# Kernel tuning notes

Measured on AMD Instinct MI355X. Metric: run time of the kernel, lower is better.

Reference implementation:

```python
import jax, jax.numpy as jnp
import numpy as np

N = 50000      # nodes (single coalesced node type)
IN = 256       # in_dim
H = 8          # attention heads
D = 64         # hidden_dim (per-head out dim)
HD = H * D     # 512, fused feature dim
OUT = 64       # final out_dim
M = 2          # meta-paths
E = 800000     # edges per meta-path graph
SEM_HID = 128  # SemanticAttention hidden size (DGL/OpenHGNN default)
NEG_SLOPE = 0.2


def setup_inputs() -> dict:
    key = jax.random.key(0)
    ks = jax.random.split(key, 13)
    s = 0.05
    return {
        "x": jax.random.normal(ks[0], (N, IN), jnp.float32),
        "src": jax.random.randint(ks[1], (M, E), 0, N, jnp.int32),
        "dst": jax.random.randint(ks[2], (M, E), 0, N, jnp.int32),
        # per-metapath GATConv params
        "Wg": jax.random.normal(ks[3], (M, IN, HD), jnp.float32) * s,
        "al": jax.random.normal(ks[4], (M, H, D), jnp.float32) * s,
        "ar": jax.random.normal(ks[5], (M, H, D), jnp.float32) * s,
        "bg": jax.random.normal(ks[6], (M, HD), jnp.float32) * s,
        # semantic attention: Linear(HD,128) -> tanh -> Linear(128,1,no bias)
        "W1": jax.random.normal(ks[7], (HD, SEM_HID), jnp.float32) * s,
        "b1": jax.random.normal(ks[8], (SEM_HID,), jnp.float32) * s,
        "q": jax.random.normal(ks[9], (SEM_HID,), jnp.float32) * s,
        # final linear
        "Wout": jax.random.normal(ks[10], (HD, OUT), jnp.float32) * s,
        "bout": jax.random.normal(ks[11], (OUT,), jnp.float32) * s,
    }


def _gat(x, W, al, ar, b, src, dst):
    # x: [N, IN] -> feat: [N, H, D]
    feat = (x @ W).reshape(N, H, D)
    el = jnp.sum(feat * al, axis=-1)                      # [N, H]
    er = jnp.sum(feat * ar, axis=-1)                      # [N, H]
    e = jax.nn.leaky_relu(el[src] + er[dst], NEG_SLOPE)   # [E, H]
    # edge softmax per destination node (allow zero in-degree)
    m = jax.ops.segment_max(e, dst, num_segments=N)       # [N, H]
    m = jnp.where(jnp.isfinite(m), m, 0.0)
    ex = jnp.exp(e - m[dst])                              # [E, H]
    den = jax.ops.segment_sum(ex, dst, num_segments=N)    # [N, H]
    alpha = ex / jnp.maximum(den[dst], 1e-9)              # [E, H]
    # scatter-aggregate messages: [E, H, D] -> [N, H, D]
    out = jax.ops.segment_sum(alpha[:, :, None] * feat[src], dst, num_segments=N)
    return jax.nn.elu(out.reshape(N, HD) + b)             # flatten heads + bias + elu


def reference(x, src, dst, Wg, al, ar, bg, W1, b1, q, Wout, bout):
    # per-metapath GAT (loop over M=2 structurally distinct graphs)
    zs = [_gat(x, Wg[p], al[p], ar[p], bg[p], src[p], dst[p]) for p in range(M)]
    z = jnp.stack(zs, axis=1)                             # [N, M, HD]
    # semantic attention fusion
    w = jnp.mean(jnp.tanh(z @ W1 + b1) @ q, axis=0)       # [M]
    beta = jax.nn.softmax(w)                              # [M]
    fused = jnp.einsum("nmf,m->nf", z, beta)             # [N, HD]
    # final linear
    return fused @ Wout + bout                            # [N, OUT]
```

## Files before the change

### kernel.cpp

```cpp
#include <hip/hip_runtime.h>
#include <cstdint>

#define N_NODES 50000
#define IN_DIM 256
#define H_HEADS 8
#define D_HEAD 64
#define HD 512
#define OUT_DIM 64
#define M_PATHS 2
#define E_EDGES 800000
#define SEM_HID 128
#define NEG_SLOPE 0.2f
#define ELL_CAP 64
#define ELX_BLOCKS 782

typedef __attribute__((ext_vector_type(8))) short bf16x8;
typedef __attribute__((ext_vector_type(4))) float f32x4;
typedef __attribute__((ext_vector_type(8))) unsigned short u16x8;

__device__ __forceinline__ float b2f(unsigned short u) {
  return __uint_as_float(((unsigned)u) << 16);
}
__device__ __forceinline__ unsigned short f2b(float f) {
  unsigned u = __float_as_uint(f);
  unsigned r = (u + 0x7fffu + ((u >> 16) & 1u)) >> 16;
  return (unsigned short)r;
}

__device__ __forceinline__ float eluf(float x) {
  return x > 0.f ? x : (expf(x) - 1.f);
}
__device__ __forceinline__ float lrelu(float x) {
  return x > 0.f ? x : NEG_SLOPE * x;
}

__global__ void k_prep(const float* __restrict__ Wg, const float* __restrict__ W1,
                       const float* __restrict__ Wout, const float* __restrict__ al,
                       const float* __restrict__ ar,
                       unsigned short* __restrict__ WgbT, unsigned short* __restrict__ W1T,
                       unsigned short* __restrict__ WoutT, unsigned short* __restrict__ WALR,
                       int* __restrict__ deg2, float* __restrict__ wsem) {
  int gid = blockIdx.x * blockDim.x + threadIdx.x;
  if (gid < 262144) {
    int m = gid >> 17, r = gid & 131071, n = r >> 8, k = r & 255;
    WgbT[(size_t)m * 131072 + n * 256 + k] = f2b(Wg[(size_t)m * 131072 + k * 512 + n]);
  } else if (gid < 327680) {
    int r = gid - 262144; int c = r >> 9, k = r & 511;
    W1T[c * 512 + k] = f2b(W1[k * 128 + c]);
  } else if (gid < 360448) {
    int r = gid - 327680; int c = r >> 9, k = r & 511;
    WoutT[c * 512 + k] = f2b(Wout[k * 64 + c]);
  } else if (gid < 368640) {
    int r = gid - 360448;
    int c = r >> 8, k = r & 255;
    int m = c >> 4, side = (c >> 3) & 1, h = c & 7;
    const float* av = (side ? ar : al) + m * HD + h * D_HEAD;
    const float* wrow = Wg + (size_t)m * 131072 + (size_t)k * HD + h * D_HEAD;
    float s = 0.f;
#pragma unroll
    for (int d = 0; d < 64; ++d) s += wrow[d] * av[d];
    WALR[c * 256 + k] = f2b(s);
  } else if (gid < 468640) {
    deg2[gid - 368640] = 0;
  } else if (gid < 468642) {
    wsem[gid - 468640] = 0.f;
  }
}

__global__ __launch_bounds__(256) void k_elx_edge(const float* __restrict__ xfp,
                                                  const unsigned short* __restrict__ WALR,
                                                  unsigned short* __restrict__ xb,
                                                  float* __restrict__ el2,
                                                  float* __restrict__ er2,
                                                  const int* __restrict__ src0,
                                                  const int* __restrict__ dst0,
                                                  int* __restrict__ deg0,
                                                  unsigned short* __restrict__ ell) {
  __shared__ __align__(16) unsigned short As[64][72];
  __shared__ __align__(16) unsigned short Bs[32][72];
  const int tid = threadIdx.x;
  if (blockIdx.x >= ELX_BLOCKS) {
    int e = (blockIdx.x - ELX_BLOCKS) * 256 + tid;
    if (e < E_EDGES) {
      int d = dst0[e];
      int p = atomicAdd(&deg0[d], 1);
      if (p < ELL_CAP) ell[d * ELL_CAP + p] = (unsigned short)src0[e];
    }
    return;
  }
  const int r0 = blockIdx.x * 64;
  const int w = tid >> 6, lane = tid & 63;
  const int cl = lane & 15, kg = lane >> 4;
  f32x4 acc[2] = {};
  for (int k0 = 0; k0 < IN_DIM; k0 += 64) {
#pragma unroll
    for (int p = 0; p < 2; ++p) {
      int idx = tid + p * 256;
      int row = idx >> 3, ko = (idx & 7) * 8;
      u16x8 v = (u16x8)(unsigned short)0;
      int grow = r0 + row;
      if (grow < N_NODES) {
        const float4* g = (const float4*)&xfp[(size_t)grow * IN_DIM + k0 + ko];
        float4 g0 = g[0], g1 = g[1];
        v[0] = f2b(g0.x); v[1] = f2b(g0.y); v[2] = f2b(g0.z); v[3] = f2b(g0.w);
        v[4] = f2b(g1.x); v[5] = f2b(g1.y); v[6] = f2b(g1.z); v[7] = f2b(g1.w);
        *(u16x8*)&xb[(size_t)grow * IN_DIM + k0 + ko] = v;
      }
      *(u16x8*)&As[row][ko] = v;
    }
    {
      int col = tid >> 3, ko = (tid & 7) * 8;
      *(u16x8*)&Bs[col][ko] = *(const u16x8*)&WALR[col * 256 + k0 + ko];
    }
    __syncthreads();
#pragma unroll
    for (int kk = 0; kk < 64; kk += 32) {
      bf16x8 a = *(const bf16x8*)&As[w * 16 + cl][kk + kg * 8];
#pragma unroll
      for (int ct = 0; ct < 2; ++ct) {
        bf16x8 b = *(const bf16x8*)&Bs[ct * 16 + cl][kk + kg * 8];
        acc[ct] = __builtin_amdgcn_mfma_f32_16x16x32_bf16(a, b, acc[ct], 0, 0, 0);
      }
    }
    __syncthreads();
  }
#pragma unroll
  for (int ct = 0; ct < 2; ++ct) {
    int col = ct * 16 + cl;
    int m = col >> 4, side = (col >> 3) & 1, h = col & 7;
    float* dstp = (side ? er2 : el2) + m * 400000;
#pragma unroll
    for (int reg = 0; reg < 4; ++reg) {
      int row = r0 + w * 16 + kg * 4 + reg;
      if (row < N_NODES) dstp[row * 8 + h] = acc[ct][reg];
    }
  }
}

__global__ void k_edge_e(const int* __restrict__ src, const int* __restrict__ dst,
                         int* __restrict__ deg, unsigned short* __restrict__ ell_src) {
  int e = blockIdx.x * blockDim.x + threadIdx.x;
  if (e >= E_EDGES) return;
  int d = dst[e];
  int p = atomicAdd(&deg[d], 1);
  if (p < ELL_CAP) ell_src[d * ELL_CAP + p] = (unsigned short)src[e];
}

__global__ __launch_bounds__(256) void k_gemm_feat(const unsigned short* __restrict__ xb,
                                                   const unsigned short* __restrict__ BT,
                                                   unsigned short* __restrict__ C) {
  __shared__ __align__(16) unsigned short As[64][72];
  __shared__ __align__(16) unsigned short Bs[256][72];
  const int tid = threadIdx.x;
  const int r0 = blockIdx.x * 64, c0 = blockIdx.y * 256;
  const int w = tid >> 6, lane = tid & 63;
  const int cl = lane & 15, kg = lane >> 4;
  const int rw = (w >> 1) * 32;
  const int cw = (w & 1) * 128;
  f32x4 acc[2][8] = {};
  for (int k0 = 0; k0 < IN_DIM; k0 += 64) {
#pragma unroll
    for (int p = 0; p < 2; ++p) {
      int idx = tid + p * 256;
      int row = idx >> 3, ko = (idx & 7) * 8;
      u16x8 v = (u16x8)(unsigned short)0;
      int grow = r0 + row;
      if (grow < N_NODES) v = *(const u16x8*)&xb[(size_t)grow * IN_DIM + k0 + ko];
      *(u16x8*)&As[row][ko] = v;
    }
#pragma unroll
    for (int p = 0; p < 8; ++p) {
      int idx = tid + p * 256;
      int col = idx >> 3, ko = (idx & 7) * 8;
      *(u16x8*)&Bs[col][ko] = *(const u16x8*)&BT[(size_t)(c0 + col) * IN_DIM + k0 + ko];
    }
    __syncthreads();
#pragma unroll
    for (int kk = 0; kk < 64; kk += 32) {
      bf16x8 a0 = *(const bf16x8*)&As[rw + cl][kk + kg * 8];
      bf16x8 a1 = *(const bf16x8*)&As[rw + 16 + cl][kk + kg * 8];
#pragma unroll
      for (int ct = 0; ct < 8; ++ct) {
        bf16x8 b = *(const bf16x8*)&Bs[cw + ct * 16 + cl][kk + kg * 8];
        acc[0][ct] = __builtin_amdgcn_mfma_f32_16x16x32_bf16(a0, b, acc[0][ct], 0, 0, 0);
        acc[1][ct] = __builtin_amdgcn_mfma_f32_16x16x32_bf16(a1, b, acc[1][ct], 0, 0, 0);
      }
    }
    __syncthreads();
  }
  const int ccol = c0 + cw;
#pragma unroll
  for (int rt = 0; rt < 2; ++rt)
#pragma unroll
    for (int ct = 0; ct < 8; ++ct)
#pragma unroll
      for (int reg = 0; reg < 4; ++reg) {
        int row = r0 + rw + rt * 16 + kg * 4 + reg;
        if (row < N_NODES) C[(size_t)row * HD + ccol + ct * 16 + cl] = f2b(acc[rt][ct][reg]);
      }
}

__global__ __launch_bounds__(256) void k_agg(const unsigned short* __restrict__ featb,
                                             const float* __restrict__ el,
                                             const float* __restrict__ er,
                                             const unsigned short* __restrict__ ell_src,
                                             const int* __restrict__ deg,
                                             const float* __restrict__ bg,
                                             unsigned short* __restrict__ z) {
  __shared__ float lds_ex[4][544];
  const int tid = threadIdx.x;
  const int widx = tid >> 6, lane = tid & 63;
  const int n = blockIdx.x * 4 + widx;
  const int h = lane >> 3;
  int s_raw = (int)ell_src[n * ELL_CAP + lane];
  int dcnt_raw = deg[n];
  const float4* r4 = (const float4*)&er[n * 8];
  float4 b0 = r4[0], b1v = r4[1];
  int s_reg = s_raw;
  const float4* e4 = (const float4*)&el[s_reg * 8];
  float4 a0 = e4[0], a1 = e4[1];
  const int dcnt = min(dcnt_raw, ELL_CAP);
  const bool valid = lane < dcnt;
  float evf[8];
  evf[0] = lrelu(a0.x + b0.x); evf[1] = lrelu(a0.y + b0.y);
  evf[2] = lrelu(a0.z + b0.z); evf[3] = lrelu(a0.w + b0.w);
  evf[4] = lrelu(a1.x + b1v.x); evf[5] = lrelu(a1.y + b1v.y);
  evf[6] = lrelu(a1.z + b1v.z); evf[7] = lrelu(a1.w + b1v.w);
  if (!valid) {
#pragma unroll
    for (int j = 0; j < 8; ++j) evf[j] = -1e30f;
  }
  float mx[8];
#pragma unroll
  for (int j = 0; j < 8; ++j) mx[j] = evf[j];
#pragma unroll
  for (int off = 1; off < 64; off <<= 1)
#pragma unroll
    for (int j = 0; j < 8; ++j) mx[j] = fmaxf(mx[j], __shfl_xor(mx[j], off));
#pragma unroll
  for (int j = 0; j < 8; ++j) {
    float exv = valid ? expf(evf[j] - mx[j]) : 0.f;
    lds_ex[widx][j * 68 + lane] = exv;
  }
  float acc[8] = {};
  float densum = 0.f;
  const float* exrow = &lds_ex[widx][h * 68];
  const unsigned short* fb = featb + lane * 8;
  int i = 0;
  for (; i + 8 <= dcnt; i += 8) {
    int ss[8];
    float ww[8];
    u16x8 ff[8];
#pragma unroll
    for (int u = 0; u < 8; ++u) {
      ss[u] = __shfl(s_reg, i + u);
      ww[u] = exrow[i + u];
    }
#pragma unroll
    for (int u = 0; u < 8; ++u) ff[u] = *(const u16x8*)&fb[(size_t)ss[u] * HD];
#pragma unroll
    for (int u = 0; u < 8; ++u) {
      densum += ww[u];
#pragma unroll
      for (int j = 0; j < 8; ++j) acc[j] += ww[u] * b2f(ff[u][j]);
    }
  }
  for (; i + 4 <= dcnt; i += 4) {
    int ss[4];
    float ww[4];
    u16x8 ff[4];
#pragma unroll
    for (int u = 0; u < 4; ++u) {
      ss[u] = __shfl(s_reg, i + u);
      ww[u] = exrow[i + u];
    }
#pragma unroll
    for (int u = 0; u < 4; ++u) ff[u] = *(const u16x8*)&fb[(size_t)ss[u] * HD];
#pragma unroll
    for (int u = 0; u < 4; ++u) {
      densum += ww[u];
#pragma unroll
      for (int j = 0; j < 8; ++j) acc[j] += ww[u] * b2f(ff[u][j]);
    }
  }
  for (; i < dcnt; ++i) {
    int s0 = __shfl(s_reg, i);
    float w0 = exrow[i];
    u16x8 f0 = *(const u16x8*)&fb[(size_t)s0 * HD];
    densum += w0;
#pragma unroll
    for (int j = 0; j < 8; ++j) acc[j] += w0 * b2f(f0[j]);
  }
  float ds = 1.f / fmaxf(densum, 1e-9f);
  const float4* bg4 = (const float4*)&bg[lane * 8];
  float4 bga = bg4[0], bgb = bg4[1];
  float bgv[8] = {bga.x, bga.y, bga.z, bga.w, bgb.x, bgb.y, bgb.z, bgb.w};
  u16x8 zo;
#pragma unroll
  for (int j = 0; j < 8; ++j) zo[j] = f2b(eluf(acc[j] * ds + bgv[j]));
  *(u16x8*)&z[(size_t)n * HD + lane * 8] = zo;
}

__global__ __launch_bounds__(256) void k_gemm_post(const unsigned short* __restrict__ Zb,
                                                   const unsigned short* __restrict__ W1T,
                                                   const unsigned short* __restrict__ WoutT,
                                                   const float* __restrict__ b1,
                                                   const float* __restrict__ qv,
                                                   float* __restrict__ wsem_m,
                                                   unsigned short* __restrict__ yb) {
  __shared__ __align__(16) unsigned short As[128][72];
  __shared__ __align__(16) unsigned short Bs[192][72];
  __shared__ float redv[16];
  const int tid = threadIdx.x;
  const int r0 = blockIdx.x * 128;
  const int w = tid >> 6, lane = tid & 63;
  const int cl = lane & 15, kg = lane >> 4;
  const int rw = w * 32;
  f32x4 acc[2][12] = {};
  for (int k0 = 0; k0 < HD; k0 += 64) {
#pragma unroll
    for (int p = 0; p < 4; ++p) {
      int idx = tid + p * 256;
      int row = idx >> 3, ko = (idx & 7) * 8;
      u16x8 v = (u16x8)(unsigned short)0;
      if (r0 + row < N_NODES) v = *(const u16x8*)&Zb[(size_t)(r0 + row) * HD + k0 + ko];
      *(u16x8*)&As[row][ko] = v;
    }
#pragma unroll
    for (int p = 0; p < 6; ++p) {
      int idx = tid + p * 256;
      int col = idx >> 3, ko = (idx & 7) * 8;
      u16x8 v = (col < 128) ? *(const u16x8*)&W1T[(size_t)col * HD + k0 + ko]
                            : *(const u16x8*)&WoutT[(size_t)(col - 128) * HD + k0 + ko];
      *(u16x8*)&Bs[col][ko] = v;
    }
    __syncthreads();
#pragma unroll
    for (int kk = 0; kk < 64; kk += 32) {
      bf16x8 a0 = *(const bf16x8*)&As[rw + cl][kk + kg * 8];
      bf16x8 a1 = *(const bf16x8*)&As[rw + 16 + cl][kk + kg * 8];
#pragma unroll
      for (int ct = 0; ct < 12; ++ct) {
        bf16x8 b = *(const bf16x8*)&Bs[ct * 16 + cl][kk + kg * 8];
        acc[0][ct] = __builtin_amdgcn_mfma_f32_16x16x32_bf16(a0, b, acc[0][ct], 0, 0, 0);
        acc[1][ct] = __builtin_amdgcn_mfma_f32_16x16x32_bf16(a1, b, acc[1][ct], 0, 0, 0);
      }
    }
    __syncthreads();
  }
  float rs[2][4] = {};
#pragma unroll
  for (int ct = 0; ct < 8; ++ct) {
    int col = ct * 16 + cl;
    float bb = b1[col], qq = qv[col];
#pragma unroll
    for (int rt = 0; rt < 2; ++rt)
#pragma unroll
      for (int reg = 0; reg < 4; ++reg)
        rs[rt][reg] += tanhf(acc[rt][ct][reg] + bb) * qq;
  }
#pragma unroll
  for (int off = 1; off < 16; off <<= 1)
#pragma unroll
    for (int rt = 0; rt < 2; ++rt)
#pragma unroll
      for (int reg = 0; reg < 4; ++reg) rs[rt][reg] += __shfl_xor(rs[rt][reg], off);
  float val = 0.f;
#pragma unroll
  for (int rt = 0; rt < 2; ++rt)
#pragma unroll
    for (int reg = 0; reg < 4; ++reg) {
      int row = r0 + rw + rt * 16 + kg * 4 + reg;
      if (row < N_NODES) val += rs[rt][reg];
    }
  if (cl == 0) redv[w * 4 + kg] = val;
  __syncthreads();
  if (tid == 0) {
    float sv = 0.f;
#pragma unroll
    for (int k = 0; k < 16; ++k) sv += redv[k];
    atomicAdd(wsem_m, sv);
  }
#pragma unroll
  for (int rt = 0; rt < 2; ++rt)
#pragma unroll
    for (int ct = 8; ct < 12; ++ct)
#pragma unroll
      for (int reg = 0; reg < 4; ++reg) {
        int row = r0 + rw + rt * 16 + kg * 4 + reg;
        if (row < N_NODES)
          yb[(size_t)row * OUT_DIM + (ct - 8) * 16 + cl] = f2b(acc[rt][ct][reg]);
      }
}

__global__ void k_final(const unsigned short* __restrict__ yb, const float* __restrict__ wsem,
                        const float* __restrict__ bout, float* __restrict__ out) {
  int gid = blockIdx.x * blockDim.x + threadIdx.x;
  size_t off = (size_t)gid * 8;
  if (off >= (size_t)N_NODES * OUT_DIM) return;
  float w0 = wsem[0] / (float)N_NODES, w1 = wsem[1] / (float)N_NODES;
  float mxv = fmaxf(w0, w1);
  float e0 = expf(w0 - mxv), e1 = expf(w1 - mxv);
  float inv = 1.f / (e0 + e1);
  float b0 = e0 * inv, b1v = e1 * inv;
  u16x8 ya = *(const u16x8*)&yb[off];
  u16x8 yc = *(const u16x8*)&yb[(size_t)N_NODES * OUT_DIM + off];
  const int cb = (int)(off & 63);
#pragma unroll
  for (int j = 0; j < 8; ++j)
    out[off + j] = b0 * b2f(ya[j]) + b1v * b2f(yc[j]) + bout[cb + j];
}

extern "C" void kernel_launch(void* const* d_in, const int* in_sizes, int n_in,
                              void* d_out, int out_size, void* d_ws, size_t ws_size,
                              hipStream_t stream) {
  const float* x    = (const float*)d_in[0];
  const int*   src  = (const int*)d_in[1];
  const int*   dst  = (const int*)d_in[2];
  const float* Wg   = (const float*)d_in[3];
  const float* al   = (const float*)d_in[4];
  const float* ar   = (const float*)d_in[5];
  const float* bg   = (const float*)d_in[6];
  const float* W1   = (const float*)d_in[7];
  const float* b1   = (const float*)d_in[8];
  const float* q    = (const float*)d_in[9];
  const float* Wout = (const float*)d_in[10];
  const float* bout = (const float*)d_in[11];
  float* out = (float*)d_out;

  char* ws = (char*)d_ws;
  unsigned short* featb = (unsigned short*)(ws);
  unsigned short* z     = (unsigned short*)(ws + 51200000);
  unsigned short* yb    = (unsigned short*)(ws + 102400000);
  unsigned short* xb    = (unsigned short*)(ws + 115200000);
  unsigned short* ell   = (unsigned short*)(ws + 140800000);
  float* el2            = (float*)(ws + 147200000);
  float* er2            = (float*)(ws + 150400000);
  int* deg2             = (int*)(ws + 153600000);
  unsigned short* WgbT  = (unsigned short*)(ws + 154000000);
  unsigned short* W1T   = (unsigned short*)(ws + 154524288);
  unsigned short* WoutT = (unsigned short*)(ws + 154655360);
  unsigned short* WALR  = (unsigned short*)(ws + 154720896);
  float* wsem           = (float*)(ws + 154737280);

  k_prep<<<1831, 256, 0, stream>>>(Wg, W1, Wout, al, ar, WgbT, W1T, WoutT, WALR,
                                   deg2, wsem);
  k_elx_edge<<<ELX_BLOCKS + 3125, 256, 0, stream>>>(x, WALR, xb, el2, er2,
                                                    src, dst, deg2, ell);

  for (int m = 0; m < M_PATHS; ++m) {
    dim3 gf(782, 2);
    k_gemm_feat<<<gf, 256, 0, stream>>>(xb, WgbT + (size_t)m * 131072, featb);
    k_agg<<<12500, 256, 0, stream>>>(featb, el2 + m * 400000, er2 + m * 400000,
                                     ell, deg2 + m * N_NODES, bg + m * HD, z);
    k_gemm_post<<<391, 256, 0, stream>>>(z, W1T, WoutT, b1, q, wsem + m,
                                         yb + (size_t)m * N_NODES * OUT_DIM);
    if (m == 0) {
      k_edge_e<<<3125, 256, 0, stream>>>(src + E_EDGES, dst + E_EDGES,
                                         deg2 + N_NODES, ell);
    }
  }
  k_final<<<1563, 256, 0, stream>>>(yb, wsem, bout, out);
}
```

Baseline: 537.4 us.

## Fuse cross-metapath stages into heterogeneous kernels to overlap aggregation with GEMMs

```diff
diff --git a/kernel.cpp b/kernel.cpp
--- a/kernel.cpp
+++ b/kernel.cpp
@@ -33,6 +33,263 @@
 __device__ __forceinline__ float lrelu(float x) {
   return x > 0.f ? x : NEG_SLOPE * x;
 }
+
+
+__device__ __forceinline__ void dev_edge(const int* __restrict__ src,
+                                         const int* __restrict__ dst,
+                                         int* __restrict__ deg,
+                                         unsigned short* __restrict__ ell, int bx) {
+  int e = bx * 256 + threadIdx.x;
+  if (e >= E_EDGES) return;
+  int d = dst[e];
+  int p = atomicAdd(&deg[d], 1);
+  if (p < ELL_CAP) ell[d * ELL_CAP + p] = (unsigned short)src[e];
+}
+
+__device__ void dev_gemm_feat(char* smem, const unsigned short* __restrict__ xb,
+                              const unsigned short* __restrict__ BT,
+                              unsigned short* __restrict__ C, int bx, int by) {
+  unsigned short (*As)[72] = (unsigned short (*)[72])smem;
+  unsigned short (*Bs)[72] = (unsigned short (*)[72])(smem + 9216);
+  const int tid = threadIdx.x;
+  const int r0 = bx * 64, c0 = by * 256;
+  const int w = tid >> 6, lane = tid & 63;
+  const int cl = lane & 15, kg = lane >> 4;
+  const int rw = (w >> 1) * 32;
+  const int cw = (w & 1) * 128;
+  f32x4 acc[2][8] = {};
+  for (int k0 = 0; k0 < IN_DIM; k0 += 64) {
+#pragma unroll
+    for (int p = 0; p < 2; ++p) {
+      int idx = tid + p * 256;
+      int row = idx >> 3, ko = (idx & 7) * 8;
+      u16x8 v = (u16x8)(unsigned short)0;
+      int grow = r0 + row;
+      if (grow < N_NODES) v = *(const u16x8*)&xb[(size_t)grow * IN_DIM + k0 + ko];
+      *(u16x8*)&As[row][ko] = v;
+    }
+#pragma unroll
+    for (int p = 0; p < 8; ++p) {
+      int idx = tid + p * 256;
+      int col = idx >> 3, ko = (idx & 7) * 8;
+      *(u16x8*)&Bs[col][ko] = *(const u16x8*)&BT[(size_t)(c0 + col) * IN_DIM + k0 + ko];
+    }
+    __syncthreads();
+#pragma unroll
+    for (int kk = 0; kk < 64; kk += 32) {
+      bf16x8 a0 = *(const bf16x8*)&As[rw + cl][kk + kg * 8];
+      bf16x8 a1 = *(const bf16x8*)&As[rw + 16 + cl][kk + kg * 8];
+#pragma unroll
+      for (int ct = 0; ct < 8; ++ct) {
+        bf16x8 b = *(const bf16x8*)&Bs[cw + ct * 16 + cl][kk + kg * 8];
+        acc[0][ct] = __builtin_amdgcn_mfma_f32_16x16x32_bf16(a0, b, acc[0][ct], 0, 0, 0);
+        acc[1][ct] = __builtin_amdgcn_mfma_f32_16x16x32_bf16(a1, b, acc[1][ct], 0, 0, 0);
+      }
+    }
+    __syncthreads();
+  }
+  const int ccol = c0 + cw;
+#pragma unroll
+  for (int rt = 0; rt < 2; ++rt)
+#pragma unroll
+    for (int ct = 0; ct < 8; ++ct)
+#pragma unroll
+      for (int reg = 0; reg < 4; ++reg) {
+        int row = r0 + rw + rt * 16 + kg * 4 + reg;
+        if (row < N_NODES) C[(size_t)row * HD + ccol + ct * 16 + cl] = f2b(acc[rt][ct][reg]);
+      }
+}
+
+__device__ void dev_agg(char* smem, const unsigned short* __restrict__ featb,
+                        const float* __restrict__ el, const float* __restrict__ er,
+                        const unsigned short* __restrict__ ell_src,
+                        const int* __restrict__ deg, const float* __restrict__ bg,
+                        unsigned short* __restrict__ z, int bx) {
+  float (*lds_ex)[544] = (float (*)[544])smem;
+  const int tid = threadIdx.x;
+  const int widx = tid >> 6, lane = tid & 63;
+  const int n = bx * 4 + widx;
+  const int h = lane >> 3;
+  int s_raw = (int)ell_src[n * ELL_CAP + lane];
+  int dcnt_raw = deg[n];
+  const float4* r4 = (const float4*)&er[n * 8];
+  float4 b0 = r4[0], b1v = r4[1];
+  int s_reg = s_raw;
+  const float4* e4 = (const float4*)&el[s_reg * 8];
+  float4 a0 = e4[0], a1 = e4[1];
+  const int dcnt = min(dcnt_raw, ELL_CAP);
+  const bool valid = lane < dcnt;
+  float evf[8];
+  evf[0] = lrelu(a0.x + b0.x); evf[1] = lrelu(a0.y + b0.y);
+  evf[2] = lrelu(a0.z + b0.z); evf[3] = lrelu(a0.w + b0.w);
+  evf[4] = lrelu(a1.x + b1v.x); evf[5] = lrelu(a1.y + b1v.y);
+  evf[6] = lrelu(a1.z + b1v.z); evf[7] = lrelu(a1.w + b1v.w);
+  if (!valid) {
+#pragma unroll
+    for (int j = 0; j < 8; ++j) evf[j] = -1e30f;
+  }
+  float mx[8];
+#pragma unroll
+  for (int j = 0; j < 8; ++j) mx[j] = evf[j];
+#pragma unroll
+  for (int off = 1; off < 64; off <<= 1)
+#pragma unroll
+    for (int j = 0; j < 8; ++j) mx[j] = fmaxf(mx[j], __shfl_xor(mx[j], off));
+#pragma unroll
+  for (int j = 0; j < 8; ++j) {
+    float exv = valid ? expf(evf[j] - mx[j]) : 0.f;
+    lds_ex[widx][j * 68 + lane] = exv;
+  }
+  float acc[8] = {};
+  float densum = 0.f;
+  const float* exrow = &lds_ex[widx][h * 68];
+  const unsigned short* fb = featb + lane * 8;
+  int i = 0;
+  for (; i + 8 <= dcnt; i += 8) {
+    int ss[8];
+    float ww[8];
+    u16x8 ff[8];
+#pragma unroll
+    for (int u = 0; u < 8; ++u) {
+      ss[u] = __shfl(s_reg, i + u);
+      ww[u] = exrow[i + u];
+    }
+#pragma unroll
+    for (int u = 0; u < 8; ++u) ff[u] = *(const u16x8*)&fb[(size_t)ss[u] * HD];
+#pragma unroll
+    for (int u = 0; u < 8; ++u) {
+      densum += ww[u];
+#pragma unroll
+      for (int j = 0; j < 8; ++j) acc[j] += ww[u] * b2f(ff[u][j]);
+    }
+  }
+  for (; i + 4 <= dcnt; i += 4) {
+    int ss[4];
+    float ww[4];
+    u16x8 ff[4];
+#pragma unroll
+    for (int u = 0; u < 4; ++u) {
+      ss[u] = __shfl(s_reg, i + u);
+      ww[u] = exrow[i + u];
+    }
+#pragma unroll
+    for (int u = 0; u < 4; ++u) ff[u] = *(const u16x8*)&fb[(size_t)ss[u] * HD];
+#pragma unroll
+    for (int u = 0; u < 4; ++u) {
+      densum += ww[u];
+#pragma unroll
+      for (int j = 0; j < 8; ++j) acc[j] += ww[u] * b2f(ff[u][j]);
+    }
+  }
+  for (; i < dcnt; ++i) {
+    int s0 = __shfl(s_reg, i);
+    float w0 = exrow[i];
+    u16x8 f0 = *(const u16x8*)&fb[(size_t)s0 * HD];
+    densum += w0;
+#pragma unroll
+    for (int j = 0; j < 8; ++j) acc[j] += w0 * b2f(f0[j]);
+  }
+  float ds = 1.f / fmaxf(densum, 1e-9f);
+  const float4* bg4 = (const float4*)&bg[lane * 8];
+  float4 bga = bg4[0], bgb = bg4[1];
+  float bgv[8] = {bga.x, bga.y, bga.z, bga.w, bgb.x, bgb.y, bgb.z, bgb.w};
+  u16x8 zo;
+#pragma unroll
+  for (int j = 0; j < 8; ++j) zo[j] = f2b(eluf(acc[j] * ds + bgv[j]));
+  *(u16x8*)&z[(size_t)n * HD + lane * 8] = zo;
+}
+
+__device__ void dev_gemm_post(char* smem, const unsigned short* __restrict__ Zb,
+                              const unsigned short* __restrict__ W1T,
+                              const unsigned short* __restrict__ WoutT,
+                              const float* __restrict__ b1, const float* __restrict__ qv,
+                              float* __restrict__ wsem_m,
+                              unsigned short* __restrict__ yb, int bx) {
+  unsigned short (*As)[72] = (unsigned short (*)[72])smem;
+  unsigned short (*Bs)[72] = (unsigned short (*)[72])(smem + 18432);
+  float* redv = (float*)(smem + 46080);
+  const int tid = threadIdx.x;
+  const int r0 = bx * 128;
+  const int w = tid >> 6, lane = tid & 63;
+  const int cl = lane & 15, kg = lane >> 4;
+  const int rw = w * 32;
+  f32x4 acc[2][12] = {};
+  for (int k0 = 0; k0 < HD; k0 += 64) {
+#pragma unroll
+    for (int p = 0; p < 4; ++p) {
+      int idx = tid + p * 256;
+      int row = idx >> 3, ko = (idx & 7) * 8;
+      u16x8 v = (u16x8)(unsigned short)0;
+      if (r0 + row < N_NODES) v = *(const u16x8*)&Zb[(size_t)(r0 + row) * HD + k0 + ko];
+      *(u16x8*)&As[row][ko] = v;
+    }
+#pragma unroll
+    for (int p = 0; p < 6; ++p) {
+      int idx = tid + p * 256;
+      int col = idx >> 3, ko = (idx & 7) * 8;
+      u16x8 v = (col < 128) ? *(const u16x8*)&W1T[(size_t)col * HD + k0 + ko]
+                            : *(const u16x8*)&WoutT[(size_t)(col - 128) * HD + k0 + ko];
+      *(u16x8*)&Bs[col][ko] = v;
+    }
+    __syncthreads();
+#pragma unroll
+    for (int kk = 0; kk < 64; kk += 32) {
+      bf16x8 a0 = *(const bf16x8*)&As[rw + cl][kk + kg * 8];
+      bf16x8 a1 = *(const bf16x8*)&As[rw + 16 + cl][kk + kg * 8];
+#pragma unroll
+      for (int ct = 0; ct < 12; ++ct) {
+        bf16x8 b = *(const bf16x8*)&Bs[ct * 16 + cl][kk + kg * 8];
+        acc[0][ct] = __builtin_amdgcn_mfma_f32_16x16x32_bf16(a0, b, acc[0][ct], 0, 0, 0);
+        acc[1][ct] = __builtin_amdgcn_mfma_f32_16x16x32_bf16(a1, b, acc[1][ct], 0, 0, 0);
+      }
+    }
+    __syncthreads();
+  }
+  float rs[2][4] = {};
+#pragma unroll
+  for (int ct = 0; ct < 8; ++ct) {
+    int col = ct * 16 + cl;
+    float bb = b1[col], qq = qv[col];
+#pragma unroll
+    for (int rt = 0; rt < 2; ++rt)
+#pragma unroll
+      for (int reg = 0; reg < 4; ++reg)
+        rs[rt][reg] += tanhf(acc[rt][ct][reg] + bb) * qq;
+  }
+#pragma unroll
+  for (int off = 1; off < 16; off <<= 1)
+#pragma unroll
+    for (int rt = 0; rt < 2; ++rt)
+#pragma unroll
+      for (int reg = 0; reg < 4; ++reg) rs[rt][reg] += __shfl_xor(rs[rt][reg], off);
+  float val = 0.f;
+#pragma unroll
+  for (int rt = 0; rt < 2; ++rt)
+#pragma unroll
+    for (int reg = 0; reg < 4; ++reg) {
+      int row = r0 + rw + rt * 16 + kg * 4 + reg;
+      if (row < N_NODES) val += rs[rt][reg];
+    }
+  if (cl == 0) redv[w * 4 + kg] = val;
+  __syncthreads();
+  if (tid == 0) {
+    float sv = 0.f;
+#pragma unroll
+    for (int k = 0; k < 16; ++k) sv += redv[k];
+    atomicAdd(wsem_m, sv);
+  }
+#pragma unroll
+  for (int rt = 0; rt < 2; ++rt)
+#pragma unroll
+    for (int ct = 8; ct < 12; ++ct)
+#pragma unroll
+      for (int reg = 0; reg < 4; ++reg) {
+        int row = r0 + rw + rt * 16 + kg * 4 + reg;
+        if (row < N_NODES)
+          yb[(size_t)row * OUT_DIM + (ct - 8) * 16 + cl] = f2b(acc[rt][ct][reg]);
+      }
+}
+
 
 __global__ void k_prep(const float* __restrict__ Wg, const float* __restrict__ W1,
                        const float* __restrict__ Wout, const float* __restrict__ al,
@@ -80,12 +337,7 @@
   __shared__ __align__(16) unsigned short Bs[32][72];
   const int tid = threadIdx.x;
   if (blockIdx.x >= ELX_BLOCKS) {
-    int e = (blockIdx.x - ELX_BLOCKS) * 256 + tid;
-    if (e < E_EDGES) {
-      int d = dst0[e];
-      int p = atomicAdd(&deg0[d], 1);
-      if (p < ELL_CAP) ell[d * ELL_CAP + p] = (unsigned short)src0[e];
-    }
+    dev_edge(src0, dst0, deg0, ell, blockIdx.x - ELX_BLOCKS);
     return;
   }
   const int r0 = blockIdx.x * 64;
@@ -137,67 +389,18 @@
   }
 }
 
-__global__ void k_edge_e(const int* __restrict__ src, const int* __restrict__ dst,
-                         int* __restrict__ deg, unsigned short* __restrict__ ell_src) {
-  int e = blockIdx.x * blockDim.x + threadIdx.x;
-  if (e >= E_EDGES) return;
-  int d = dst[e];
-  int p = atomicAdd(&deg[d], 1);
-  if (p < ELL_CAP) ell_src[d * ELL_CAP + p] = (unsigned short)src[e];
+__global__ __launch_bounds__(256) void k_edge(const int* __restrict__ src,
+                                              const int* __restrict__ dst,
+                                              int* __restrict__ deg,
+                                              unsigned short* __restrict__ ell) {
+  dev_edge(src, dst, deg, ell, blockIdx.x);
 }
 
 __global__ __launch_bounds__(256) void k_gemm_feat(const unsigned short* __restrict__ xb,
                                                    const unsigned short* __restrict__ BT,
                                                    unsigned short* __restrict__ C) {
-  __shared__ __align__(16) unsigned short As[64][72];
-  __shared__ __align__(16) unsigned short Bs[256][72];
-  const int tid = threadIdx.x;
-  const int r0 = blockIdx.x * 64, c0 = blockIdx.y * 256;
-  const int w = tid >> 6, lane = tid & 63;
-  const int cl = lane & 15, kg = lane >> 4;
-  const int rw = (w >> 1) * 32;
-  const int cw = (w & 1) * 128;
-  f32x4 acc[2][8] = {};
-  for (int k0 = 0; k0 < IN_DIM; k0 += 64) {
-#pragma unroll
-    for (int p = 0; p < 2; ++p) {
-      int idx = tid + p * 256;
-      int row = idx >> 3, ko = (idx & 7) * 8;
-      u16x8 v = (u16x8)(unsigned short)0;
-      int grow = r0 + row;
-      if (grow < N_NODES) v = *(const u16x8*)&xb[(size_t)grow * IN_DIM + k0 + ko];
-      *(u16x8*)&As[row][ko] = v;
-    }
-#pragma unroll
-    for (int p = 0; p < 8; ++p) {
-      int idx = tid + p * 256;
-      int col = idx >> 3, ko = (idx & 7) * 8;
-      *(u16x8*)&Bs[col][ko] = *(const u16x8*)&BT[(size_t)(c0 + col) * IN_DIM + k0 + ko];
-    }
-    __syncthreads();
-#pragma unroll
-    for (int kk = 0; kk < 64; kk += 32) {
-      bf16x8 a0 = *(const bf16x8*)&As[rw + cl][kk + kg * 8];
-      bf16x8 a1 = *(const bf16x8*)&As[rw + 16 + cl][kk + kg * 8];
-#pragma unroll
-      for (int ct = 0; ct < 8; ++ct) {
-        bf16x8 b = *(const bf16x8*)&Bs[cw + ct * 16 + cl][kk + kg * 8];
-        acc[0][ct] = __builtin_amdgcn_mfma_f32_16x16x32_bf16(a0, b, acc[0][ct], 0, 0, 0);
-        acc[1][ct] = __builtin_amdgcn_mfma_f32_16x16x32_bf16(a1, b, acc[1][ct], 0, 0, 0);
-      }
-    }
-    __syncthreads();
-  }
-  const int ccol = c0 + cw;
-#pragma unroll
-  for (int rt = 0; rt < 2; ++rt)
-#pragma unroll
-    for (int ct = 0; ct < 8; ++ct)
-#pragma unroll
-      for (int reg = 0; reg < 4; ++reg) {
-        int row = r0 + rw + rt * 16 + kg * 4 + reg;
-        if (row < N_NODES) C[(size_t)row * HD + ccol + ct * 16 + cl] = f2b(acc[rt][ct][reg]);
-      }
+  __shared__ __align__(16) char smem[46080];
+  dev_gemm_feat(smem, xb, BT, C, blockIdx.x, blockIdx.y);
 }
 
 __global__ __launch_bounds__(256) void k_agg(const unsigned short* __restrict__ featb,
@@ -207,98 +410,8 @@
                                              const int* __restrict__ deg,
                                              const float* __restrict__ bg,
                                              unsigned short* __restrict__ z) {
-  __shared__ float lds_ex[4][544];
-  const int tid = threadIdx.x;
-  const int widx = tid >> 6, lane = tid & 63;
-  const int n = blockIdx.x * 4 + widx;
-  const int h = lane >> 3;
-  int s_raw = (int)ell_src[n * ELL_CAP + lane];
-  int dcnt_raw = deg[n];
-  const float4* r4 = (const float4*)&er[n * 8];
-  float4 b0 = r4[0], b1v = r4[1];
-  int s_reg = s_raw;
-  const float4* e4 = (const float4*)&el[s_reg * 8];
-  float4 a0 = e4[0], a1 = e4[1];
-  const int dcnt = min(dcnt_raw, ELL_CAP);
-  const bool valid = lane < dcnt;
-  float evf[8];
-  evf[0] = lrelu(a0.x + b0.x); evf[1] = lrelu(a0.y + b0.y);
-  evf[2] = lrelu(a0.z + b0.z); evf[3] = lrelu(a0.w + b0.w);
-  evf[4] = lrelu(a1.x + b1v.x); evf[5] = lrelu(a1.y + b1v.y);
-  evf[6] = lrelu(a1.z + b1v.z); evf[7] = lrelu(a1.w + b1v.w);
-  if (!valid) {
-#pragma unroll
-    for (int j = 0; j < 8; ++j) evf[j] = -1e30f;
-  }
-  float mx[8];
-#pragma unroll
-  for (int j = 0; j < 8; ++j) mx[j] = evf[j];
-#pragma unroll
-  for (int off = 1; off < 64; off <<= 1)
-#pragma unroll
-    for (int j = 0; j < 8; ++j) mx[j] = fmaxf(mx[j], __shfl_xor(mx[j], off));
-#pragma unroll
-  for (int j = 0; j < 8; ++j) {
-    float exv = valid ? expf(evf[j] - mx[j]) : 0.f;
-    lds_ex[widx][j * 68 + lane] = exv;
-  }
-  float acc[8] = {};
-  float densum = 0.f;
-  const float* exrow = &lds_ex[widx][h * 68];
-  const unsigned short* fb = featb + lane * 8;
-  int i = 0;
-  for (; i + 8 <= dcnt; i += 8) {
-    int ss[8];
-    float ww[8];
-    u16x8 ff[8];
-#pragma unroll
-    for (int u = 0; u < 8; ++u) {
-      ss[u] = __shfl(s_reg, i + u);
-      ww[u] = exrow[i + u];
-    }
-#pragma unroll
-    for (int u = 0; u < 8; ++u) ff[u] = *(const u16x8*)&fb[(size_t)ss[u] * HD];
-#pragma unroll
-    for (int u = 0; u < 8; ++u) {
-      densum += ww[u];
-#pragma unroll
-      for (int j = 0; j < 8; ++j) acc[j] += ww[u] * b2f(ff[u][j]);
-    }
-  }
-  for (; i + 4 <= dcnt; i += 4) {
-    int ss[4];
-    float ww[4];
-    u16x8 ff[4];
-#pragma unroll
-    for (int u = 0; u < 4; ++u) {
-      ss[u] = __shfl(s_reg, i + u);
-      ww[u] = exrow[i + u];
-    }
-#pragma unroll
-    for (int u = 0; u < 4; ++u) ff[u] = *(const u16x8*)&fb[(size_t)ss[u] * HD];
-#pragma unroll
-    for (int u = 0; u < 4; ++u) {
-      densum += ww[u];
-#pragma unroll
-      for (int j = 0; j < 8; ++j) acc[j] += ww[u] * b2f(ff[u][j]);
-    }
-  }
-  for (; i < dcnt; ++i) {
-    int s0 = __shfl(s_reg, i);
-    float w0 = exrow[i];
-    u16x8 f0 = *(const u16x8*)&fb[(size_t)s0 * HD];
-    densum += w0;
-#pragma unroll
-    for (int j = 0; j < 8; ++j) acc[j] += w0 * b2f(f0[j]);
-  }
-  float ds = 1.f / fmaxf(densum, 1e-9f);
-  const float4* bg4 = (const float4*)&bg[lane * 8];
-  float4 bga = bg4[0], bgb = bg4[1];
-  float bgv[8] = {bga.x, bga.y, bga.z, bga.w, bgb.x, bgb.y, bgb.z, bgb.w};
-  u16x8 zo;
-#pragma unroll
-  for (int j = 0; j < 8; ++j) zo[j] = f2b(eluf(acc[j] * ds + bgv[j]));
-  *(u16x8*)&z[(size_t)n * HD + lane * 8] = zo;
+  __shared__ __align__(16) char smem[8704];
+  dev_agg(smem, featb, el, er, ell_src, deg, bg, z, blockIdx.x);
 }
 
 __global__ __launch_bounds__(256) void k_gemm_post(const unsigned short* __restrict__ Zb,
@@ -308,89 +421,50 @@
                                                    const float* __restrict__ qv,
                                                    float* __restrict__ wsem_m,
                                                    unsigned short* __restrict__ yb) {
-  __shared__ __align__(16) unsigned short As[128][72];
-  __shared__ __align__(16) unsigned short Bs[192][72];
-  __shared__ float redv[16];
-  const int tid = threadIdx.x;
-  const int r0 = blockIdx.x * 128;
-  const int w = tid >> 6, lane = tid & 63;
-  const int cl = lane & 15, kg = lane >> 4;
-  const int rw = w * 32;
-  f32x4 acc[2][12] = {};
-  for (int k0 = 0; k0 < HD; k0 += 64) {
-#pragma unroll
-    for (int p = 0; p < 4; ++p) {
-      int idx = tid + p * 256;
-      int row = idx >> 3, ko = (idx & 7) * 8;
-      u16x8 v = (u16x8)(unsigned short)0;
-      if (r0 + row < N_NODES) v = *(const u16x8*)&Zb[(size_t)(r0 + row) * HD + k0 + ko];
-      *(u16x8*)&As[row][ko] = v;
-    }
-#pragma unroll
-    for (int p = 0; p < 6; ++p) {
-      int idx = tid + p * 256;
-      int col = idx >> 3, ko = (idx & 7) * 8;
-      u16x8 v = (col < 128) ? *(const u16x8*)&W1T[(size_t)col * HD + k0 + ko]
-                            : *(const u16x8*)&WoutT[(size_t)(col - 128) * HD + k0 + ko];
-      *(u16x8*)&Bs[col][ko] = v;
-    }
-    __syncthreads();
-#pragma unroll
-    for (int kk = 0; kk < 64; kk += 32) {
-      bf16x8 a0 = *(const bf16x8*)&As[rw + cl][kk + kg * 8];
-      bf16x8 a1 = *(const bf16x8*)&As[rw + 16 + cl][kk + kg * 8];
-#pragma unroll
-      for (int ct = 0; ct < 12; ++ct) {
-        bf16x8 b = *(const bf16x8*)&Bs[ct * 16 + cl][kk + kg * 8];
-        acc[0][ct] = __builtin_amdgcn_mfma_f32_16x16x32_bf16(a0, b, acc[0][ct], 0, 0, 0);
-        acc[1][ct] = __builtin_amdgcn_mfma_f32_16x16x32_bf16(a1, b, acc[1][ct], 0, 0, 0);
-      }
-    }
-    __syncthreads();
-  }
-  float rs[2][4] = {};
-#pragma unroll
-  for (int ct = 0; ct < 8; ++ct) {
-    int col = ct * 16 + cl;
-    float bb = b1[col], qq = qv[col];
-#pragma unroll
-    for (int rt = 0; rt < 2; ++rt)
-#pragma unroll
-      for (int reg = 0; reg < 4; ++reg)
-        rs[rt][reg] += tanhf(acc[rt][ct][reg] + bb) * qq;
-  }
-#pragma unroll
-  for (int off = 1; off < 16; off <<= 1)
-#pragma unroll
-    for (int rt = 0; rt < 2; ++rt)
-#pragma unroll
-      for (int reg = 0; reg < 4; ++reg) rs[rt][reg] += __shfl_xor(rs[rt][reg], off);
-  float val = 0.f;
-#pragma unroll
-  for (int rt = 0; rt < 2; ++rt)
-#pragma unroll
-    for (int reg = 0; reg < 4; ++reg) {
-      int row = r0 + rw + rt * 16 + kg * 4 + reg;
-      if (row < N_NODES) val += rs[rt][reg];
-    }
-  if (cl == 0) redv[w * 4 + kg] = val;
-  __syncthreads();
-  if (tid == 0) {
-    float sv = 0.f;
-#pragma unroll
-    for (int k = 0; k < 16; ++k) sv += redv[k];
-    atomicAdd(wsem_m, sv);
-  }
-#pragma unroll
-  for (int rt = 0; rt < 2; ++rt)
-#pragma unroll
-    for (int ct = 8; ct < 12; ++ct)
-#pragma unroll
-      for (int reg = 0; reg < 4; ++reg) {
-        int row = r0 + rw + rt * 16 + kg * 4 + reg;
-        if (row < N_NODES)
-          yb[(size_t)row * OUT_DIM + (ct - 8) * 16 + cl] = f2b(acc[rt][ct][reg]);
-      }
+  __shared__ __align__(16) char smem[46144];
+  dev_gemm_post(smem, Zb, W1T, WoutT, b1, qv, wsem_m, yb, blockIdx.x);
+}
+
+__global__ __launch_bounds__(256) void k_fused1(
+    const unsigned short* __restrict__ featb0, const float* __restrict__ el0,
+    const float* __restrict__ er0, const unsigned short* __restrict__ ell0,
+    const int* __restrict__ deg0, const float* __restrict__ bg0,
+    unsigned short* __restrict__ z0,
+    const unsigned short* __restrict__ xb, const unsigned short* __restrict__ BT1,
+    unsigned short* __restrict__ featb1,
+    const int* __restrict__ src1, const int* __restrict__ dst1,
+    int* __restrict__ deg1, unsigned short* __restrict__ ell1) {
+  __shared__ __align__(16) char smem[46080];
+  const int bid = blockIdx.x;
+  const int g = bid / 11, r = bid - g * 11;
+  if (r < 8) {
+    int ai = g * 8 + r;
+    if (ai < 12500) dev_agg(smem, featb0, el0, er0, ell0, deg0, bg0, z0, ai);
+  } else {
+    int xi = g * 3 + (r - 8);
+    if (xi < 1564) dev_gemm_feat(smem, xb, BT1, featb1, xi % 782, xi / 782);
+    else if (xi < 4689) dev_edge(src1, dst1, deg1, ell1, xi - 1564);
+  }
+}
+
+__global__ __launch_bounds__(256) void k_fused2(
+    const unsigned short* __restrict__ featb1, const float* __restrict__ el1,
+    const float* __restrict__ er1, const unsigned short* __restrict__ ell1,
+    const int* __restrict__ deg1, const float* __restrict__ bg1,
+    unsigned short* __restrict__ z1,
+    const unsigned short* __restrict__ z0, const unsigned short* __restrict__ W1T,
+    const unsigned short* __restrict__ WoutT, const float* __restrict__ b1,
+    const float* __restrict__ qv, float* __restrict__ wsem0,
+    unsigned short* __restrict__ yb0) {
+  __shared__ __align__(16) char smem[46144];
+  const int bid = blockIdx.x;
+  const int g = bid / 33, r = bid - g * 33;
+  if (r < 32) {
+    int ai = g * 32 + r;
+    if (ai < 12500) dev_agg(smem, featb1, el1, er1, ell1, deg1, bg1, z1, ai);
+  } else {
+    if (g < 391) dev_gemm_post(smem, z0, W1T, WoutT, b1, qv, wsem0, yb0, g);
+  }
 }
 
 __global__ void k_final(const unsigned short* __restrict__ yb, const float* __restrict__ wsem,
@@ -427,38 +501,75 @@
   const float* Wout = (const float*)d_in[10];
   const float* bout = (const float*)d_in[11];
   float* out = (float*)d_out;
-
   char* ws = (char*)d_ws;
-  unsigned short* featb = (unsigned short*)(ws);
-  unsigned short* z     = (unsigned short*)(ws + 51200000);
-  unsigned short* yb    = (unsigned short*)(ws + 102400000);
-  unsigned short* xb    = (unsigned short*)(ws + 115200000);
-  unsigned short* ell   = (unsigned short*)(ws + 140800000);
-  float* el2            = (float*)(ws + 147200000);
-  float* er2            = (float*)(ws + 150400000);
-  int* deg2             = (int*)(ws + 153600000);
-  unsigned short* WgbT  = (unsigned short*)(ws + 154000000);
-  unsigned short* W1T   = (unsigned short*)(ws + 154524288);
-  unsigned short* WoutT = (unsigned short*)(ws + 154655360);
-  unsigned short* WALR  = (unsigned short*)(ws + 154720896);
-  float* wsem           = (float*)(ws + 154737280);
-
-  k_prep<<<1831, 256, 0, stream>>>(Wg, W1, Wout, al, ar, WgbT, W1T, WoutT, WALR,
-                                   deg2, wsem);
-  k_elx_edge<<<ELX_BLOCKS + 3125, 256, 0, stream>>>(x, WALR, xb, el2, er2,
-                                                    src, dst, deg2, ell);
-
-  for (int m = 0; m < M_PATHS; ++m) {
+
+  const size_t NEED_FULL = 199537408;
+
+  if (ws_size >= NEED_FULL) {
+    unsigned short* featb0 = (unsigned short*)(ws);
+    unsigned short* z1     = (unsigned short*)(ws);
+    unsigned short* featb1 = (unsigned short*)(ws + 51200000);
+    unsigned short* z0     = (unsigned short*)(ws + 102400000);
+    unsigned short* xb     = (unsigned short*)(ws + 153600000);
+    unsigned short* yb     = (unsigned short*)(ws + 153600000);
+    unsigned short* ell0   = (unsigned short*)(ws + 179200000);
+    unsigned short* ell1   = (unsigned short*)(ws + 185600000);
+    float* el2             = (float*)(ws + 192000000);
+    float* er2             = (float*)(ws + 195200000);
+    int* deg2              = (int*)(ws + 198400000);
+    unsigned short* WgbT   = (unsigned short*)(ws + 198800000);
+    unsigned short* W1T    = (unsigned short*)(ws + 199324288);
+    unsigned short* WoutT  = (unsigned short*)(ws + 199455360);
+    unsigned short* WALR   = (unsigned short*)(ws + 199520896);
+    float* wsem            = (float*)(ws + 199537280);
+
+    k_prep<<<1831, 256, 0, stream>>>(Wg, W1, Wout, al, ar, WgbT, W1T, WoutT, WALR,
+                                     deg2, wsem);
+    k_elx_edge<<<ELX_BLOCKS + 3125, 256, 0, stream>>>(x, WALR, xb, el2, er2,
+                                                      src, dst, deg2, ell0);
     dim3 gf(782, 2);
-    k_gemm_feat<<<gf, 256, 0, stream>>>(xb, WgbT + (size_t)m * 131072, featb);
-    k_agg<<<12500, 256, 0, stream>>>(featb, el2 + m * 400000, er2 + m * 400000,
-                                     ell, deg2 + m * N_NODES, bg + m * HD, z);
-    k_gemm_post<<<391, 256, 0, stream>>>(z, W1T, WoutT, b1, q, wsem + m,
-                                         yb + (size_t)m * N_NODES * OUT_DIM);
-    if (m == 0) {
-      k_edge_e<<<3125, 256, 0, stream>>>(src + E_EDGES, dst + E_EDGES,
+    k_gemm_feat<<<gf, 256, 0, stream>>>(xb, WgbT, featb0);
+    k_fused1<<<17193, 256, 0, stream>>>(featb0, el2, er2, ell0, deg2, bg, z0,
+                                        xb, WgbT + 131072, featb1,
+                                        src + E_EDGES, dst + E_EDGES,
+                                        deg2 + N_NODES, ell1);
+    k_fused2<<<12903, 256, 0, stream>>>(featb1, el2 + 400000, er2 + 400000, ell1,
+                                        deg2 + N_NODES, bg + HD, z1,
+                                        z0, W1T, WoutT, b1, q, wsem, yb);
+    k_gemm_post<<<391, 256, 0, stream>>>(z1, W1T, WoutT, b1, q, wsem + 1,
+                                         yb + (size_t)N_NODES * OUT_DIM);
+    k_final<<<1563, 256, 0, stream>>>(yb, wsem, bout, out);
+  } else {
+    unsigned short* featb = (unsigned short*)(ws);
+    unsigned short* z     = (unsigned short*)(ws + 51200000);
+    unsigned short* yb    = (unsigned short*)(ws + 102400000);
+    unsigned short* xb    = (unsigned short*)(ws + 115200000);
+    unsigned short* ell   = (unsigned short*)(ws + 140800000);
+    float* el2            = (float*)(ws + 147200000);
+    float* er2            = (float*)(ws + 150400000);
+    int* deg2             = (int*)(ws + 153600000);
+    unsigned short* WgbT  = (unsigned short*)(ws + 154000000);
+    unsigned short* W1T   = (unsigned short*)(ws + 154524288);
+    unsigned short* WoutT = (unsigned short*)(ws + 154655360);
+    unsigned short* WALR  = (unsigned short*)(ws + 154720896);
+    float* wsem           = (float*)(ws + 154737280);
+
+    k_prep<<<1831, 256, 0, stream>>>(Wg, W1, Wout, al, ar, WgbT, W1T, WoutT, WALR,
+                                     deg2, wsem);
+    k_elx_edge<<<ELX_BLOCKS + 3125, 256, 0, stream>>>(x, WALR, xb, el2, er2,
+                                                      src, dst, deg2, ell);
+    for (int m = 0; m < M_PATHS; ++m) {
+      dim3 gf(782, 2);
+      k_gemm_feat<<<gf, 256, 0, stream>>>(xb, WgbT + (size_t)m * 131072, featb);
+      k_agg<<<12500, 256, 0, stream>>>(featb, el2 + m * 400000, er2 + m * 400000,
+                                       ell, deg2 + m * N_NODES, bg + m * HD, z);
+      k_gemm_post<<<391, 256, 0, stream>>>(z, W1T, WoutT, b1, q, wsem + m,
+                                           yb + (size_t)m * N_NODES * OUT_DIM);
+      if (m == 0) {
+        k_edge<<<3125, 256, 0, stream>>>(src + E_EDGES, dst + E_EDGES,
                                          deg2 + N_NODES, ell);
-    }
-  }
-  k_final<<<1563, 256, 0, stream>>>(yb, wsem, bout, out);
-}
+      }
+    }
+    k_final<<<1563, 256, 0, stream>>>(yb, wsem, bout, out);
+  }
+}
```

Measured after the change: 1.043 ms. 94.0% more time.
